# Performance work log

Measured on AMD Instinct MI355X. Metric: run time of the kernel, lower is better.

The kernel has to match this reference:

```python
import jax, jax.numpy as jnp
import numpy as np

B, T = 64, 512
OBS, DM, DS, NL = 115, 128, 8, 3
EMB, NA, H1 = 16, 19, 256


def _ln(x, g, b, eps=1e-5):
    m = jnp.mean(x, -1, keepdims=True)
    v = jnp.mean((x - m) ** 2, -1, keepdims=True)
    return (x - m) * jax.lax.rsqrt(v + eps) * g + b


def _s6(x, h, lng, lnb, w_ig, w_dt, b_dt, a_log, w_b, w_c, d_par, w_out):
    # x: [B,T,DM], h: [B,DM,DS]
    xn = _ln(x, lng, lnb)
    xp = xn @ w_ig.T                               # [B,T,2*DM]
    x_in, z = xp[..., :DM], xp[..., DM:]
    dt = jax.nn.softplus(x_in @ w_dt.T + b_dt)     # [B,T,DM]
    A = -jnp.exp(a_log)                            # [DM,DS]
    bt = x_in @ w_b.T                              # [B,T,DS]
    ct = x_in @ w_c.T                              # [B,T,DS]
    dA = jnp.exp(dt[..., None] * A)                # [B,T,DM,DS]
    upd = (dt * x_in)[..., None] * bt[:, :, None, :]  # [B,T,DM,DS]

    def step(hc, inp):
        dA_t, u_t, c_t = inp
        hn = dA_t * hc + u_t                       # [B,DM,DS]
        y = jnp.einsum('bds,bs->bd', hn, c_t)      # [B,DM]
        return hn, y

    h_f, ys = jax.lax.scan(
        step, h,
        (jnp.swapaxes(dA, 0, 1), jnp.swapaxes(upd, 0, 1), jnp.swapaxes(ct, 0, 1)))
    y = jnp.swapaxes(ys, 0, 1)                     # [B,T,DM]
    ssm = y * jax.nn.silu(z) + x_in * d_par
    return x + ssm @ w_out.T, h_f.reshape(h_f.shape[0], -1)


def _forward(prev_actions, obs, h0, enc_w1, enc_b1, enc_g1, enc_bb1, enc_w2, enc_b2,
             enc_g2, enc_bb2, emb, proj_w, proj_b, proj_g, proj_bb,
             m_ln_g, m_ln_b, m_w_ig, m_w_dt, m_b_dt, m_a_log, m_w_b, m_w_c, m_d, m_w_out,
             fn_g, fn_b, pol_w1, pol_b1, pol_g, pol_bb, pol_w2, pol_b2):
    # MLP encoder: Linear -> LN -> SiLU -> Linear -> LN (final norm)
    e = jax.nn.silu(_ln(obs @ enc_w1.T + enc_b1, enc_g1, enc_bb1))
    e = _ln(e @ enc_w2.T + enc_b2, enc_g2, enc_bb2)
    pa = emb[prev_actions]                         # [B,T,EMB]
    x = jnp.concatenate([e, pa], -1) @ proj_w.T + proj_b
    x = jax.nn.silu(_ln(x, proj_g, proj_bb))
    for i in range(NL):
        x, _ = _s6(x, h0[i].reshape(-1, DM, DS), m_ln_g[i], m_ln_b[i], m_w_ig[i],
                   m_w_dt[i], m_b_dt[i], m_a_log[i], m_w_b[i], m_w_c[i], m_d[i], m_w_out[i])
    x = _ln(x, fn_g, fn_b)
    p = jax.nn.silu(_ln(x @ pol_w1.T + pol_b1, pol_g, pol_bb))
    return p @ pol_w2.T + pol_b2                   # [B,T,NA] policy logits


def setup_inputs() -> dict:
    key = jax.random.key(0)
    ks = iter(jax.random.split(key, 64))
    def n(shape, s=0.05):
        return jax.random.normal(next(ks), shape, dtype=jnp.float32) * s
    return {
        'obs': jax.random.normal(next(ks), (B, T, OBS), dtype=jnp.float32),
        'h0': jnp.zeros((NL, B, DM * DS), jnp.float32),
        'enc_w1': n((H1, OBS)), 'enc_b1': jnp.zeros((H1,)),
        'enc_g1': jnp.ones((H1,)), 'enc_bb1': jnp.zeros((H1,)),
        'enc_w2': n((DM, H1)), 'enc_b2': jnp.zeros((DM,)),
        'enc_g2': jnp.ones((DM,)), 'enc_bb2': jnp.zeros((DM,)),
        'emb': n((NA + 1, EMB), 1.0),
        'proj_w': n((DM, DM + EMB)), 'proj_b': jnp.zeros((DM,)),
        'proj_g': jnp.ones((DM,)), 'proj_bb': jnp.zeros((DM,)),
        'm_ln_g': jnp.ones((NL, DM)), 'm_ln_b': jnp.zeros((NL, DM)),
        'm_w_ig': n((NL, 2 * DM, DM)), 'm_w_dt': n((NL, DM, DM)),
        'm_b_dt': jnp.zeros((NL, DM)),
        'm_a_log': jax.random.uniform(next(ks), (NL, DM, DS), minval=-3.0, maxval=-1.0, dtype=jnp.float32),
        'm_w_b': n((NL, DS, DM)), 'm_w_c': n((NL, DS, DM)),
        'm_d': jnp.ones((NL, DM)), 'm_w_out': n((NL, DM, DM)),
        'fn_g': jnp.ones((DM,)), 'fn_b': jnp.zeros((DM,)),
        'pol_w1': n((DM, DM)), 'pol_b1': jnp.zeros((DM,)),
        'pol_g': jnp.ones((DM,)), 'pol_bb': jnp.zeros((DM,)),
        'pol_w2': n((NA, DM)), 'pol_b2': jnp.zeros((NA,)),
        'prev_actions': jax.random.randint(next(ks), (B, T), 0, NA + 1),
    }


def reference(obs, h0, enc_w1, enc_b1, enc_g1, enc_bb1, enc_w2, enc_b2, enc_g2, enc_bb2,
              emb, proj_w, proj_b, proj_g, proj_bb, m_ln_g, m_ln_b, m_w_ig, m_w_dt,
              m_b_dt, m_a_log, m_w_b, m_w_c, m_d, m_w_out, fn_g, fn_b, pol_w1, pol_b1,
              pol_g, pol_bb, pol_w2, pol_b2, prev_actions):
    return _forward(prev_actions, obs, h0, enc_w1, enc_b1, enc_g1, enc_bb1, enc_w2,
                    enc_b2, enc_g2, enc_bb2, emb, proj_w, proj_b, proj_g, proj_bb,
                    m_ln_g, m_ln_b, m_w_ig, m_w_dt, m_b_dt, m_a_log, m_w_b, m_w_c,
                    m_d, m_w_out, fn_g, fn_b, pol_w1, pol_b1, pol_g, pol_bb, pol_w2, pol_b2)
```

## Files before the change

kernel.cpp:

```cpp
#include <hip/hip_runtime.h>
#include <math.h>

#define BB 64
#define TT 512
#define OBSD 115
#define DMD 128
#define DSD 8
#define NLD 3
#define EMBD 16
#define NAD 19
#define H1D 256
#define NTOK (BB*TT)
#define SSEG 32
#define TSEG (TT/SSEG)

typedef unsigned short ushort_t;
typedef __attribute__((ext_vector_type(8))) short short8;
typedef __attribute__((ext_vector_type(4))) float f32x4;

__device__ __forceinline__ float silu_f(float x){ return x / (1.f + __expf(-x)); }
__device__ __forceinline__ float softplus_f(float x){
  return fmaxf(x, 0.f) + log1pf(__expf(-fabsf(x)));
}
__device__ __forceinline__ ushort_t f2bf(float x){
  unsigned u = __float_as_uint(x);
  unsigned r = (u + 0x7fffu + ((u >> 16) & 1u)) >> 16;
  return (ushort_t)r;
}
__device__ __forceinline__ float b2f(ushort_t x){
  return __uint_as_float(((unsigned)x) << 16);
}
#define MFMA(a,b,c) __builtin_amdgcn_mfma_f32_16x16x32_bf16((a),(b),(c),0,0,0)
#define LOG2E 1.44269504f

template<int D, int SV>
__device__ __forceinline__ void ln32(const float* s_val, float* s_mr, int tid){
  const int t = tid >> 3, part = tid & 7;
  float s = 0.f, s2 = 0.f;
  #pragma unroll
  for (int j = part; j < D; j += 8){ float v = s_val[t*SV + j]; s += v; s2 = fmaf(v, v, s2); }
  s += __shfl_xor(s, 1, 64); s2 += __shfl_xor(s2, 1, 64);
  s += __shfl_xor(s, 2, 64); s2 += __shfl_xor(s2, 2, 64);
  s += __shfl_xor(s, 4, 64); s2 += __shfl_xor(s2, 4, 64);
  if (part == 0){
    float m = s * (1.f/(float)D);
    s_mr[t*2] = m;
    s_mr[t*2+1] = rsqrtf(s2 * (1.f/(float)D) - m*m + 1e-5f);
  }
}

struct PJob { const float* src; ushort_t* dst; int N; int K; int Kpad; int rowofs; int Nw; };
struct PJobs { PJob j[20]; };

__global__ __launch_bounds__(256) void k_prep(PJobs P){
  const int job = blockIdx.x >> 2;
  const int sub = blockIdx.x & 3;
  PJob pj = P.j[job];
  const int elems = pj.Nw * pj.Kpad;
  for (int idx = sub*256 + threadIdx.x; idx < elems; idx += 4*256){
    int n = idx / pj.Kpad;
    int k = idx - n*pj.Kpad;
    float v = (n < pj.N && k < pj.K) ? pj.src[(size_t)n*pj.K + k] : 0.f;
    pj.dst[(size_t)(pj.rowofs + n)*pj.Kpad + k] = f2bf(v);
  }
}

__global__ __launch_bounds__(256) void k_enc1(
    const float* __restrict__ obs, const ushort_t* __restrict__ w1b,
    const float* __restrict__ b1, const float* __restrict__ g1,
    const float* __restrict__ bb1, ushort_t* __restrict__ e1)
{
  __shared__ __align__(16) char sm[34048];
  float*    s_val = (float*)sm;
  ushort_t* s_a   = (ushort_t*)sm;
  float*    s_mr  = (float*)(sm + 33792);
  const int tok0 = blockIdx.x * 32;
  const int tid = threadIdx.x;
  const int lane = tid & 63, w = tid >> 6;
  const int q = lane >> 4, cn = lane & 15;
  const int m0 = (w & 1) * 16, nh = w >> 1;

  for (int e = tid; e < 32*16; e += 256){
    int t = e >> 4, kc = e & 15;
    const float* op = obs + (size_t)(tok0 + t)*OBSD;
    short8 v;
    #pragma unroll
    for (int j = 0; j < 8; j++){
      int k = kc*8 + j;
      v[j] = (short)f2bf(k < OBSD ? op[k] : 0.f);
    }
    *(short8*)&s_a[t*136 + kc*8] = v;
  }
  __syncthreads();

  short8 af[4];
  #pragma unroll
  for (int ks = 0; ks < 4; ks++)
    af[ks] = *(const short8*)&s_a[(m0 + cn)*136 + ks*32 + q*8];
  __syncthreads();

  #pragma unroll
  for (int nt = 0; nt < 8; nt++){
    const int n0 = (nh*8 + nt) * 16;
    f32x4 acc = {0.f,0.f,0.f,0.f};
    #pragma unroll
    for (int ks = 0; ks < 4; ks++){
      short8 bf = *(const short8*)&w1b[(size_t)(n0 + cn)*128 + ks*32 + q*8];
      acc = MFMA(af[ks], bf, acc);
    }
    float bias = b1[n0 + cn];
    #pragma unroll
    for (int r = 0; r < 4; r++)
      s_val[(m0 + q*4 + r)*264 + n0 + cn] = acc[r] + bias;
  }
  __syncthreads();

  ln32<256,264>(s_val, s_mr, tid);
  __syncthreads();
  for (int e = tid; e < 32*256; e += 256){
    int t = e >> 8, c = e & 255;
    float v = (s_val[t*264 + c] - s_mr[t*2]) * s_mr[t*2+1] * g1[c] + bb1[c];
    e1[(size_t)(tok0 + t)*256 + c] = f2bf(silu_f(v));
  }
}

__global__ __launch_bounds__(256) void k_enc2p(
    const ushort_t* __restrict__ e1, const ushort_t* __restrict__ w2b,
    const float* __restrict__ b2, const float* __restrict__ g2,
    const float* __restrict__ bb2,
    const float* __restrict__ emb, const int* __restrict__ pact,
    const ushort_t* __restrict__ pwb, const float* __restrict__ pb,
    const float* __restrict__ pg, const float* __restrict__ pbb,
    float* __restrict__ X,
    const float* __restrict__ lng, const float* __restrict__ lnb,
    const ushort_t* __restrict__ wigb, const ushort_t* __restrict__ wdbcb,
    const float* __restrict__ bdt,
    ushort_t* __restrict__ XINb, ushort_t* __restrict__ Zb,
    ushort_t* __restrict__ DTb, ushort_t* __restrict__ BTu, ushort_t* __restrict__ CTu,
    const float* __restrict__ alog0,
    float* __restrict__ HLOC, float* __restrict__ PPR)
{
  __shared__ __align__(16) char sm[28928];
  float*    s_val = (float*)sm;
  ushort_t* s_xin = (ushort_t*)sm;
  ushort_t* s_dt  = (ushort_t*)(sm + 8704);
  ushort_t* s_a   = (ushort_t*)(sm + 17408);
  ushort_t* s_btc = (ushort_t*)(sm + 28160);
  float*    s_mr  = (float*)(sm + 28672);

  const int tok0 = blockIdx.x * 32;
  const int bidx = blockIdx.x >> 4;
  const int ch   = blockIdx.x & 15;
  const int tid = threadIdx.x;
  const int lane = tid & 63, w = tid >> 6;
  const int q = lane >> 4, cn = lane & 15;
  const int m0 = (w & 1) * 16, nh = w >> 1;

  for (int e = tid; e < 32*32; e += 256){
    int t = e >> 5, k = e & 31;
    float v = 0.f;
    if (k < EMBD){ int a = pact[tok0 + t]; v = emb[(size_t)a*EMBD + k]; }
    s_a[t*168 + 128 + k] = f2bf(v);
  }
  {
    short8 af[8];
    #pragma unroll
    for (int ks = 0; ks < 8; ks++)
      af[ks] = *(const short8*)&e1[(size_t)(tok0 + m0 + cn)*256 + ks*32 + q*8];
    #pragma unroll
    for (int nt = 0; nt < 4; nt++){
      const int n0 = (nh*4 + nt) * 16;
      f32x4 acc = {0.f,0.f,0.f,0.f};
      #pragma unroll
      for (int ks = 0; ks < 8; ks++){
        short8 bf = *(const short8*)&w2b[(size_t)(n0 + cn)*256 + ks*32 + q*8];
        acc = MFMA(af[ks], bf, acc);
      }
      float bias = b2[n0 + cn];
      #pragma unroll
      for (int r = 0; r < 4; r++)
        s_val[(m0 + q*4 + r)*136 + n0 + cn] = acc[r] + bias;
    }
  }
  __syncthreads();

  ln32<128,136>(s_val, s_mr, tid);
  __syncthreads();
  for (int e = tid; e < 32*128; e += 256){
    int t = e >> 7, c = e & 127;
    float v = (s_val[t*136 + c] - s_mr[t*2]) * s_mr[t*2+1] * g2[c] + bb2[c];
    s_a[t*168 + c] = f2bf(v);
  }
  __syncthreads();

  {
    short8 af2[5];
    #pragma unroll
    for (int ks = 0; ks < 5; ks++)
      af2[ks] = *(const short8*)&s_a[(m0 + cn)*168 + ks*32 + q*8];
    #pragma unroll
    for (int nt = 0; nt < 4; nt++){
      const int n0 = (nh*4 + nt) * 16;
      f32x4 acc = {0.f,0.f,0.f,0.f};
      #pragma unroll
      for (int ks = 0; ks < 5; ks++){
        short8 bf = *(const short8*)&pwb[(size_t)(n0 + cn)*160 + ks*32 + q*8];
        acc = MFMA(af2[ks], bf, acc);
      }
      float bias = pb[n0 + cn];
      #pragma unroll
      for (int r = 0; r < 4; r++)
        s_val[(m0 + q*4 + r)*136 + n0 + cn] = acc[r] + bias;
    }
  }
  __syncthreads();

  ln32<128,136>(s_val, s_mr, tid);
  __syncthreads();
  for (int e = tid; e < 32*128; e += 256){
    int t = e >> 7, c = e & 127;
    float v = (s_val[t*136 + c] - s_mr[t*2]) * s_mr[t*2+1] * pg[c] + pbb[c];
    v = silu_f(v);
    X[(size_t)tok0*128 + e] = v;
    s_val[t*136 + c] = v;
  }
  __syncthreads();

  ln32<128,136>(s_val, s_mr, tid);
  __syncthreads();
  for (int e = tid; e < 32*128; e += 256){
    int t = e >> 7, c = e & 127;
    float v = (s_val[t*136 + c] - s_mr[t*2]) * s_mr[t*2+1] * lng[c] + lnb[c];
    s_a[t*168 + c] = f2bf(v);
  }
  __syncthreads();

  {
    short8 af[4];
    #pragma unroll
    for (int ks = 0; ks < 4; ks++)
      af[ks] = *(const short8*)&s_a[(m0 + cn)*168 + ks*32 + q*8];
    #pragma unroll
    for (int nt = 0; nt < 8; nt++){
      const int n0 = (nh*8 + nt) * 16;
      f32x4 acc = {0.f,0.f,0.f,0.f};
      #pragma unroll
      for (int ks = 0; ks < 4; ks++){
        short8 bf = *(const short8*)&wigb[(size_t)(n0 + cn)*128 + ks*32 + q*8];
        acc = MFMA(af[ks], bf, acc);
      }
      if (n0 < 128){
        #pragma unroll
        for (int r = 0; r < 4; r++){
          int tr = m0 + q*4 + r;
          ushort_t bb = f2bf(acc[r]);
          XINb[(size_t)(tok0 + tr)*128 + n0 + cn] = bb;
          s_xin[tr*136 + n0 + cn] = bb;
        }
      } else {
        #pragma unroll
        for (int r = 0; r < 4; r++){
          int tr = m0 + q*4 + r;
          Zb[(size_t)(tok0 + tr)*128 + (n0 - 128) + cn] = f2bf(acc[r]);
        }
      }
    }
  }
  __syncthreads();

  {
    short8 af2[4];
    #pragma unroll
    for (int ks = 0; ks < 4; ks++)
      af2[ks] = *(const short8*)&s_xin[(m0 + cn)*136 + ks*32 + q*8];
    for (int nt = nh; nt < 9; nt += 2){
      const int n0 = nt * 16;
      f32x4 acc = {0.f,0.f,0.f,0.f};
      #pragma unroll
      for (int ks = 0; ks < 4; ks++){
        short8 bf = *(const short8*)&wdbcb[(size_t)(n0 + cn)*128 + ks*32 + q*8];
        acc = MFMA(af2[ks], bf, acc);
      }
      const int col = n0 + cn;
      if (col < 128){
        float bd = bdt[col];
        #pragma unroll
        for (int r = 0; r < 4; r++){
          int tr = m0 + q*4 + r;
          ushort_t dv = f2bf(softplus_f(acc[r] + bd));
          DTb[(size_t)(tok0 + tr)*128 + col] = dv;
          s_dt[tr*136 + col] = dv;
        }
      } else if (col < 136){
        #pragma unroll
        for (int r = 0; r < 4; r++){
          int tr = m0 + q*4 + r;
          ushort_t bb = f2bf(acc[r]);
          BTu[(size_t)(tok0 + tr)*8 + (col - 128)] = bb;
          s_btc[tr*8 + (col - 128)] = bb;
        }
      } else {
        #pragma unroll
        for (int r = 0; r < 4; r++)
          CTu[(size_t)(tok0 + m0 + q*4 + r)*8 + (col - 136)] = f2bf(acc[r]);
      }
    }
  }
  __syncthreads();

  {
    const int d = tid & 127, half = tid >> 7;
    float A2c[8], hh[8], pp[8];
    #pragma unroll
    for (int s = 0; s < 8; s++){
      A2c[s] = -__expf(alog0[d*8 + s]) * LOG2E;
      hh[s] = 0.f; pp[s] = 1.f;
    }
    const int t0 = half * 16;
    #pragma unroll 4
    for (int tt = 0; tt < 16; tt++){
      const int t = t0 + tt;
      float dt = b2f(s_dt[t*136 + d]);
      float wv = dt * b2f(s_xin[t*136 + d]);
      #pragma unroll
      for (int s = 0; s < 8; s++){
        float dA = exp2f(dt * A2c[s]);
        hh[s] = fmaf(dA, hh[s], wv * b2f(s_btc[t*8 + s]));
        pp[s] *= dA;
      }
    }
    const size_t o = ((size_t)bidx*SSEG + ch*2 + half)*1024 + d*8;
    #pragma unroll
    for (int s = 0; s < 8; s++){ HLOC[o+s] = hh[s]; PPR[o+s] = pp[s]; }
  }
}

__global__ __launch_bounds__(256) void k_carry(
    float* __restrict__ HL, const float* __restrict__ PP,
    const float* __restrict__ h0g)
{
  const int idx = blockIdx.x*256 + threadIdx.x;
  float h = h0g[idx];
  size_t o = (size_t)(idx >> 10) * (SSEG*1024) + (idx & 1023);
  #pragma unroll 4
  for (int ch = 0; ch < SSEG; ch++){
    float hl = HL[o];
    float pp = PP[o];
    HL[o] = h;
    h = fmaf(pp, h, hl);
    o += 1024;
  }
}

#define SMB 26368

__device__ __forceinline__ void phaseB32(
    const ushort_t* DTb, const ushort_t* XINb, const ushort_t* Zb,
    const ushort_t* BTu, const ushort_t* CTu,
    const float* __restrict__ alog, const float* __restrict__ HLpre,
    const float* __restrict__ dpar, const ushort_t* __restrict__ woutb,
    float* __restrict__ X, char* sm, int b, int pair, int tid)
{
  ushort_t* s_dtS = (ushort_t*)sm;
  ushort_t* s_xiS = (ushort_t*)(sm + 8192);
  float*    s_x   = (float*)sm;
  ushort_t* s_a   = (ushort_t*)(sm + 16384);
  ushort_t* s_bt  = (ushort_t*)(sm + 25088);
  ushort_t* s_ct  = (ushort_t*)(sm + 25600);
  float*    s_mr  = (float*)(sm + 26112);

  const int lane = tid & 63, w = tid >> 6, q = lane >> 4, cn = lane & 15;
  const int m0 = (w & 1) * 16, nh = w >> 1;
  const int d = tid & 127, half = tid >> 7;
  const size_t segtok = (size_t)b*TT + pair*32;

  {
    const uint4* gdt = (const uint4*)(DTb + segtok*128);
    const uint4* gxi = (const uint4*)(XINb + segtok*128);
    #pragma unroll
    for (int i = 0; i < 2; i++){
      ((uint4*)s_dtS)[tid + i*256] = gdt[tid + i*256];
      ((uint4*)s_xiS)[tid + i*256] = gxi[tid + i*256];
    }
    if (tid < 128){
      ((unsigned*)s_bt)[tid] = ((const unsigned*)(BTu + segtok*8))[tid];
      ((unsigned*)s_ct)[tid] = ((const unsigned*)(CTu + segtok*8))[tid];
    }
  }
  float A2[8], h[8];
  {
    const size_t o = ((size_t)b*SSEG + pair*2 + half)*1024 + d*8;
    float4 h0v = *(const float4*)(HLpre + o);
    float4 h1v = *(const float4*)(HLpre + o + 4);
    h[0]=h0v.x; h[1]=h0v.y; h[2]=h0v.z; h[3]=h0v.w;
    h[4]=h1v.x; h[5]=h1v.y; h[6]=h1v.z; h[7]=h1v.w;
    #pragma unroll
    for (int s = 0; s < 8; s++) A2[s] = -__expf(alog[d*8 + s]) * LOG2E;
  }
  __syncthreads();

  #pragma unroll 4
  for (int tt = 0; tt < 16; tt++){
    const int t = half*16 + tt;
    float dt = b2f(s_dtS[t*128 + d]);
    float xi = b2f(s_xiS[t*128 + d]);
    float wv = dt * xi;
    float y = 0.f;
    #pragma unroll
    for (int s = 0; s < 8; s++){
      float dA = exp2f(dt * A2[s]);
      h[s] = fmaf(dA, h[s], wv * b2f(s_bt[t*8 + s]));
      y = fmaf(h[s], b2f(s_ct[t*8 + s]), y);
    }
    s_a[t*136 + d] = f2bf(y);
  }
  __syncthreads();

  {
    const int c0 = (tid & 15)*8, trow = tid >> 4;
    float dpv[8];
    #pragma unroll
    for (int j = 0; j < 8; j++) dpv[j] = dpar[c0 + j];
    #pragma unroll
    for (int i = 0; i < 2; i++){
      const int t = trow + i*16;
      uint4 zb = ((const uint4*)(Zb + segtok*128))[tid + i*256];
      const ushort_t* zp = (const ushort_t*)&zb;
      #pragma unroll
      for (int j = 0; j < 8; j++){
        float y  = b2f(s_a[t*136 + c0 + j]);
        float xi = b2f(s_xiS[t*128 + c0 + j]);
        float ssm = y * silu_f(b2f(zp[j])) + xi * dpv[j];
        s_a[t*136 + c0 + j] = f2bf(ssm);
      }
    }
  }
  __syncthreads();

  {
    short8 af[4];
    #pragma unroll
    for (int ks = 0; ks < 4; ks++)
      af[ks] = *(const short8*)&s_a[(m0 + cn)*136 + ks*32 + q*8];
    __syncthreads();
    #pragma unroll
    for (int i = 0; i < 4; i++){
      const int n0 = (nh*4 + i) * 16;
      short8 bf[4];
      #pragma unroll
      for (int ks = 0; ks < 4; ks++)
        bf[ks] = *(const short8*)&woutb[(size_t)(n0+cn)*128 + ks*32 + q*8];
      f32x4 acc = {0.f,0.f,0.f,0.f};
      #pragma unroll
      for (int ks = 0; ks < 4; ks++) acc = MFMA(af[ks], bf[ks], acc);
      #pragma unroll
      for (int r = 0; r < 4; r++){
        const int tr = m0 + q*4 + r;
        const size_t g = (segtok + tr)*128 + n0 + cn;
        float xn = X[g] + acc[r];
        X[g] = xn;
        s_x[tr*130 + n0 + cn] = xn;
      }
    }
  }
  __syncthreads();

  {
    const int t = tid >> 3, part = tid & 7;
    float s = 0.f, s2 = 0.f;
    const float* row = s_x + t*130 + part*16;
    #pragma unroll
    for (int j = 0; j < 16; j++){ float v = row[j]; s += v; s2 = fmaf(v, v, s2); }
    s  += __shfl_xor(s, 1, 64);  s2 += __shfl_xor(s2, 1, 64);
    s  += __shfl_xor(s, 2, 64);  s2 += __shfl_xor(s2, 2, 64);
    s  += __shfl_xor(s, 4, 64);  s2 += __shfl_xor(s2, 4, 64);
    if (part == 0){
      float m = s * (1.f/128.f);
      s_mr[t*2] = m;
      s_mr[t*2+1] = rsqrtf(s2 * (1.f/128.f) - m*m + 1e-5f);
    }
  }
  __syncthreads();
}

__global__ __launch_bounds__(256, 4) void k_scan2p(
    ushort_t* DTb, ushort_t* XINb, ushort_t* Zb,
    ushort_t* BTu, ushort_t* CTu,
    const float* __restrict__ alog, const float* __restrict__ HLpre,
    const float* __restrict__ dpar, const ushort_t* __restrict__ woutb,
    float* __restrict__ X,
    const float* __restrict__ lng, const float* __restrict__ lnb,
    const ushort_t* __restrict__ wigb, const ushort_t* __restrict__ wdbcb,
    const float* __restrict__ bdt,
    const float* __restrict__ alogn,
    float* __restrict__ HLo, float* __restrict__ PPo)
{
  __shared__ __align__(16) char sm[SMB];
  const int tid = threadIdx.x;
  float*    s_x   = (float*)sm;
  ushort_t* s_xin = (ushort_t*)sm;
  ushort_t* s_dt2 = (ushort_t*)(sm + 8704);
  ushort_t* s_a   = (ushort_t*)(sm + 16384);
  ushort_t* s_btc = (ushort_t*)(sm + 25088);
  float*    s_mr  = (float*)(sm + 26112);

  const int b = blockIdx.x >> 4;
  const int pair = blockIdx.x & 15;
  const int lane = tid & 63, w = tid >> 6, q = lane >> 4, cn = lane & 15;
  const int m0 = (w & 1) * 16, nh = w >> 1;
  const int d = tid & 127, half = tid >> 7;
  const size_t segtok = (size_t)b*TT + pair*32;

  phaseB32(DTb, XINb, Zb, BTu, CTu, alog, HLpre, dpar, woutb, X, sm, b, pair, tid);

  {
    float g = lng[d], c0v = lnb[d];
    float x31 = s_x[31*130 + d];
    __syncthreads();
    #pragma unroll
    for (int tt = 0; tt < 16; tt++){
      const int t = half*16 + tt;
      float xv = (t == 31) ? x31 : s_x[t*130 + d];
      float v = (xv - s_mr[t*2]) * s_mr[t*2+1] * g + c0v;
      s_a[t*136 + d] = f2bf(v);
    }
  }
  __syncthreads();

  {
    short8 af[4];
    #pragma unroll
    for (int ks = 0; ks < 4; ks++)
      af[ks] = *(const short8*)&s_a[(m0 + cn)*136 + ks*32 + q*8];
    #pragma unroll
    for (int i = 0; i < 8; i++){
      const int n0 = (nh*8 + i) * 16;
      short8 bf[4];
      #pragma unroll
      for (int ks = 0; ks < 4; ks++)
        bf[ks] = *(const short8*)&wigb[(size_t)(n0+cn)*128 + ks*32 + q*8];
      f32x4 acc = {0.f,0.f,0.f,0.f};
      #pragma unroll
      for (int ks = 0; ks < 4; ks++) acc = MFMA(af[ks], bf[ks], acc);
      if (n0 < 128){
        #pragma unroll
        for (int r = 0; r < 4; r++){
          const int tr = m0 + q*4 + r;
          ushort_t bb = f2bf(acc[r]);
          XINb[(segtok + tr)*128 + n0 + cn] = bb;
          s_xin[tr*136 + n0 + cn] = bb;
        }
      } else {
        #pragma unroll
        for (int r = 0; r < 4; r++){
          const int tr = m0 + q*4 + r;
          Zb[(segtok + tr)*128 + (n0-128) + cn] = f2bf(acc[r]);
        }
      }
    }
  }
  __syncthreads();

  {
    short8 af2[4];
    #pragma unroll
    for (int ks = 0; ks < 4; ks++)
      af2[ks] = *(const short8*)&s_xin[(m0 + cn)*136 + ks*32 + q*8];
    for (int nt = nh; nt < 9; nt += 2){
      const int n0 = nt * 16;
      short8 bf[4];
      #pragma unroll
      for (int ks = 0; ks < 4; ks++)
        bf[ks] = *(const short8*)&wdbcb[(size_t)(n0+cn)*128 + ks*32 + q*8];
      f32x4 acc = {0.f,0.f,0.f,0.f};
      #pragma unroll
      for (int ks = 0; ks < 4; ks++) acc = MFMA(af2[ks], bf[ks], acc);
      const int col = n0 + cn;
      if (col < 128){
        float bd = bdt[col];
        #pragma unroll
        for (int r = 0; r < 4; r++){
          const int tr = m0 + q*4 + r;
          ushort_t dv = f2bf(softplus_f(acc[r] + bd));
          DTb[(segtok + tr)*128 + col] = dv;
          s_dt2[tr*136 + col] = dv;
        }
      } else if (col < 136){
        #pragma unroll
        for (int r = 0; r < 4; r++){
          const int tr = m0 + q*4 + r;
          ushort_t bb = f2bf(acc[r]);
          BTu[(segtok + tr)*8 + (col-128)] = bb;
          s_btc[tr*8 + (col-128)] = bb;
        }
      } else {
        #pragma unroll
        for (int r = 0; r < 4; r++)
          CTu[(segtok + m0 + q*4 + r)*8 + (col-136)] = f2bf(acc[r]);
      }
    }
  }
  __syncthreads();

  {
    float A2n[8], hh[8], pp[8];
    #pragma unroll
    for (int s = 0; s < 8; s++){
      A2n[s] = -__expf(alogn[d*8 + s]) * LOG2E;
      hh[s] = 0.f; pp[s] = 1.f;
    }
    #pragma unroll 4
    for (int tt = 0; tt < 16; tt++){
      const int t = half*16 + tt;
      float dt = b2f(s_dt2[t*136 + d]);
      float wv = dt * b2f(s_xin[t*136 + d]);
      #pragma unroll
      for (int s = 0; s < 8; s++){
        float dA = exp2f(dt * A2n[s]);
        hh[s] = fmaf(dA, hh[s], wv * b2f(s_btc[t*8 + s]));
        pp[s] *= dA;
      }
    }
    const size_t o = ((size_t)b*SSEG + pair*2 + half)*1024 + d*8;
    #pragma unroll
    for (int s = 0; s < 8; s++){ HLo[o+s] = hh[s]; PPo[o+s] = pp[s]; }
  }
}

__global__ __launch_bounds__(256, 4) void k_scan2h(
    const ushort_t* DTb, const ushort_t* XINb, const ushort_t* Zb,
    const ushort_t* BTu, const ushort_t* CTu,
    const float* __restrict__ alog, const float* __restrict__ HLpre,
    const float* __restrict__ dpar, const ushort_t* __restrict__ woutb,
    float* __restrict__ X,
    const float* __restrict__ fng, const float* __restrict__ fnb,
    const ushort_t* __restrict__ pw1b, const float* __restrict__ pb1,
    const float* __restrict__ pg, const float* __restrict__ pbb,
    const ushort_t* __restrict__ pw2b, const float* __restrict__ pb2,
    float* __restrict__ out)
{
  __shared__ __align__(16) char sm[SMB];
  const int tid = threadIdx.x;
  float*    s_x  = (float*)sm;
  ushort_t* s_a  = (ushort_t*)(sm + 16384);
  float*    s_mr = (float*)(sm + 26112);

  const int b = blockIdx.x >> 4;
  const int pair = blockIdx.x & 15;
  const int lane = tid & 63, w = tid >> 6, q = lane >> 4, cn = lane & 15;
  const int m0 = (w & 1) * 16, nh = w >> 1;
  const int d = tid & 127, half = tid >> 7;
  const size_t segtok = (size_t)b*TT + pair*32;

  phaseB32((ushort_t*)DTb, (ushort_t*)XINb, (ushort_t*)Zb,
           (ushort_t*)BTu, (ushort_t*)CTu, alog, HLpre,
           dpar, woutb, X, sm, b, pair, tid);

  {
    float g = fng[d], c0v = fnb[d];
    float x31 = s_x[31*130 + d];
    __syncthreads();
    #pragma unroll
    for (int tt = 0; tt < 16; tt++){
      const int t = half*16 + tt;
      float xv = (t == 31) ? x31 : s_x[t*130 + d];
      float v = (xv - s_mr[t*2]) * s_mr[t*2+1] * g + c0v;
      s_a[t*136 + d] = f2bf(v);
    }
  }
  __syncthreads();

  {
    short8 af[4];
    #pragma unroll
    for (int ks = 0; ks < 4; ks++)
      af[ks] = *(const short8*)&s_a[(m0 + cn)*136 + ks*32 + q*8];
    __syncthreads();
    #pragma unroll
    for (int i = 0; i < 4; i++){
      const int n0 = (nh*4 + i) * 16;
      short8 bf[4];
      #pragma unroll
      for (int ks = 0; ks < 4; ks++)
        bf[ks] = *(const short8*)&pw1b[(size_t)(n0+cn)*128 + ks*32 + q*8];
      float bias = pb1[n0 + cn];
      f32x4 acc = {0.f,0.f,0.f,0.f};
      #pragma unroll
      for (int ks = 0; ks < 4; ks++) acc = MFMA(af[ks], bf[ks], acc);
      #pragma unroll
      for (int r = 0; r < 4; r++)
        s_x[(m0 + q*4 + r)*130 + n0 + cn] = acc[r] + bias;
    }
  }
  __syncthreads();

  {
    const int t = tid >> 3, part = tid & 7;
    float s = 0.f, s2 = 0.f;
    const float* row = s_x + t*130 + part*16;
    #pragma unroll
    for (int j = 0; j < 16; j++){ float v = row[j]; s += v; s2 = fmaf(v, v, s2); }
    s  += __shfl_xor(s, 1, 64);  s2 += __shfl_xor(s2, 1, 64);
    s  += __shfl_xor(s, 2, 64);  s2 += __shfl_xor(s2, 2, 64);
    s  += __shfl_xor(s, 4, 64);  s2 += __shfl_xor(s2, 4, 64);
    if (part == 0){
      float m = s * (1.f/128.f);
      s_mr[t*2] = m;
      s_mr[t*2+1] = rsqrtf(s2 * (1.f/128.f) - m*m + 1e-5f);
    }
  }
  __syncthreads();

  {
    float g = pg[d], c0v = pbb[d];
    float x31 = s_x[31*130 + d];
    __syncthreads();
    #pragma unroll
    for (int tt = 0; tt < 16; tt++){
      const int t = half*16 + tt;
      float xv = (t == 31) ? x31 : s_x[t*130 + d];
      float v = (xv - s_mr[t*2]) * s_mr[t*2+1] * g + c0v;
      s_a[t*136 + d] = f2bf(silu_f(v));
    }
  }
  __syncthreads();

  {
    short8 af[4];
    #pragma unroll
    for (int ks = 0; ks < 4; ks++)
      af[ks] = *(const short8*)&s_a[(m0 + cn)*136 + ks*32 + q*8];
    const int n0 = (w >> 1) * 16;
    short8 bf[4];
    #pragma unroll
    for (int ks = 0; ks < 4; ks++)
      bf[ks] = *(const short8*)&pw2b[(size_t)(n0+cn)*128 + ks*32 + q*8];
    const int col = n0 + cn;
    f32x4 acc = {0.f,0.f,0.f,0.f};
    #pragma unroll
    for (int ks = 0; ks < 4; ks++) acc = MFMA(af[ks], bf[ks], acc);
    if (col < NAD){
      float bias = pb2[col];
      #pragma unroll
      for (int r = 0; r < 4; r++)
        out[(segtok + m0 + q*4 + r)*NAD + col] = acc[r] + bias;
    }
  }
}

extern "C" void kernel_launch(void* const* d_in, const int* in_sizes, int n_in,
                              void* d_out, int out_size, void* d_ws, size_t ws_size,
                              hipStream_t stream) {
  const float* obs    = (const float*)d_in[0];
  const float* h0     = (const float*)d_in[1];
  const float* enc_w1 = (const float*)d_in[2];
  const float* enc_b1 = (const float*)d_in[3];
  const float* enc_g1 = (const float*)d_in[4];
  const float* enc_bb1= (const float*)d_in[5];
  const float* enc_w2 = (const float*)d_in[6];
  const float* enc_b2 = (const float*)d_in[7];
  const float* enc_g2 = (const float*)d_in[8];
  const float* enc_bb2= (const float*)d_in[9];
  const float* emb    = (const float*)d_in[10];
  const float* proj_w = (const float*)d_in[11];
  const float* proj_b = (const float*)d_in[12];
  const float* proj_g = (const float*)d_in[13];
  const float* proj_bb= (const float*)d_in[14];
  const float* m_ln_g = (const float*)d_in[15];
  const float* m_ln_b = (const float*)d_in[16];
  const float* m_w_ig = (const float*)d_in[17];
  const float* m_w_dt = (const float*)d_in[18];
  const float* m_b_dt = (const float*)d_in[19];
  const float* m_a_log= (const float*)d_in[20];
  const float* m_w_b  = (const float*)d_in[21];
  const float* m_w_c  = (const float*)d_in[22];
  const float* m_d    = (const float*)d_in[23];
  const float* m_w_out= (const float*)d_in[24];
  const float* fn_g   = (const float*)d_in[25];
  const float* fn_b   = (const float*)d_in[26];
  const float* pol_w1 = (const float*)d_in[27];
  const float* pol_b1 = (const float*)d_in[28];
  const float* pol_g  = (const float*)d_in[29];
  const float* pol_bb = (const float*)d_in[30];
  const float* pol_w2 = (const float*)d_in[31];
  const float* pol_b2 = (const float*)d_in[32];
  const int*   pact   = (const int*)d_in[33];

  float* ws  = (float*)d_ws;
  float* X    = ws;
  float* HLA  = X + (size_t)NTOK*128;
  float* PPA  = HLA + (size_t)BB*SSEG*1024;
  ushort_t* E1 = (ushort_t*)(PPA + (size_t)BB*SSEG*1024);
  float* HLB  = (float*)E1;
  float* PPB  = HLB + (size_t)BB*SSEG*1024;
  ushort_t* XINb = E1   + (size_t)NTOK*256;
  ushort_t* Zb   = XINb + (size_t)NTOK*128;
  ushort_t* DTb  = Zb   + (size_t)NTOK*128;
  ushort_t* BTu  = DTb  + (size_t)NTOK*128;
  ushort_t* CTu  = BTu  + (size_t)NTOK*8;

  ushort_t* W1B   = CTu   + (size_t)NTOK*8;
  ushort_t* W2B   = W1B   + 256*128;
  ushort_t* PWB   = W2B   + 128*256;
  ushort_t* WIGB  = PWB   + 128*160;
  ushort_t* WDBCB = WIGB  + 3*256*128;
  ushort_t* WOUTB = WDBCB + 3*144*128;
  ushort_t* PW1B  = WOUTB + 3*128*128;
  ushort_t* PW2B  = PW1B  + 128*128;

  PJobs P;
  int nj = 0;
  auto add = [&](const float* src, ushort_t* dst, int N, int K, int Kpad, int rowofs, int Nw){
    P.j[nj].src = src; P.j[nj].dst = dst; P.j[nj].N = N; P.j[nj].K = K;
    P.j[nj].Kpad = Kpad; P.j[nj].rowofs = rowofs; P.j[nj].Nw = Nw; nj++;
  };
  add(enc_w1, W1B, 256, 115, 128, 0, 256);
  add(enc_w2, W2B, 128, 256, 256, 0, 128);
  add(proj_w, PWB, 128, 144, 160, 0, 128);
  for (int l = 0; l < NLD; l++)
    add(m_w_ig + (size_t)l*256*128, WIGB + (size_t)l*256*128, 256, 128, 128, 0, 256);
  for (int l = 0; l < NLD; l++){
    add(m_w_dt + (size_t)l*128*128, WDBCB + (size_t)l*144*128, 128, 128, 128, 0,   128);
    add(m_w_b  + (size_t)l*8*128,   WDBCB + (size_t)l*144*128,   8, 128, 128, 128,   8);
    add(m_w_c  + (size_t)l*8*128,   WDBCB + (size_t)l*144*128,   8, 128, 128, 136,   8);
  }
  for (int l = 0; l < NLD; l++)
    add(m_w_out + (size_t)l*128*128, WOUTB + (size_t)l*128*128, 128, 128, 128, 0, 128);
  add(pol_w1, PW1B, 128, 128, 128, 0, 128);
  add(pol_w2, PW2B,  19, 128, 128, 0,  32);

  k_prep<<<20*4, 256, 0, stream>>>(P);
  k_enc1<<<NTOK/32, 256, 0, stream>>>(obs, W1B, enc_b1, enc_g1, enc_bb1, E1);
  k_enc2p<<<NTOK/32, 256, 0, stream>>>(E1, W2B, enc_b2, enc_g2, enc_bb2,
      emb, pact, PWB, proj_b, proj_g, proj_bb, X,
      m_ln_g, m_ln_b, WIGB, WDBCB, m_b_dt,
      XINb, Zb, DTb, BTu, CTu,
      m_a_log, HLA, PPA);

  const int carrygrid = BB*1024/256;
  const int scangrid  = NTOK/32;

  k_carry<<<carrygrid, 256, 0, stream>>>(HLA, PPA, h0);
  k_scan2p<<<scangrid, 256, 0, stream>>>(DTb, XINb, Zb, BTu, CTu,
      m_a_log, HLA, m_d, WOUTB, X,
      m_ln_g + 128, m_ln_b + 128,
      WIGB + (size_t)256*128, WDBCB + (size_t)144*128, m_b_dt + 128,
      m_a_log + 1024, HLB, PPB);
  k_carry<<<carrygrid, 256, 0, stream>>>(HLB, PPB, h0 + (size_t)BB*1024);
  k_scan2p<<<scangrid, 256, 0, stream>>>(DTb, XINb, Zb, BTu, CTu,
      m_a_log + 1024, HLB, m_d + 128, WOUTB + (size_t)128*128, X,
      m_ln_g + 256, m_ln_b + 256,
      WIGB + (size_t)2*256*128, WDBCB + (size_t)2*144*128, m_b_dt + 256,
      m_a_log + 2048, HLA, PPA);
  k_carry<<<carrygrid, 256, 0, stream>>>(HLA, PPA, h0 + (size_t)2*BB*1024);
  k_scan2h<<<scangrid, 256, 0, stream>>>(DTb, XINb, Zb, BTu, CTu,
      m_a_log + 2048, HLA, m_d + 256, WOUTB + (size_t)2*128*128, X,
      fn_g, fn_b, PW1B, pol_b1, pol_g, pol_bb, PW2B, pol_b2,
      (float*)d_out);
}
```

Measured before the change: 421.8 us.

## Fuse encoder layer one into the encoder-projection kernel and drop E1 buffer

New measurement: 409.0 us. -3.0%, faster.

```diff
diff --git a/kernel.cpp b/kernel.cpp
--- a/kernel.cpp
+++ b/kernel.cpp
@@ -65,67 +65,11 @@
   }
 }
 
-__global__ __launch_bounds__(256) void k_enc1(
+__global__ __launch_bounds__(256) void k_enc12p(
     const float* __restrict__ obs, const ushort_t* __restrict__ w1b,
     const float* __restrict__ b1, const float* __restrict__ g1,
-    const float* __restrict__ bb1, ushort_t* __restrict__ e1)
-{
-  __shared__ __align__(16) char sm[34048];
-  float*    s_val = (float*)sm;
-  ushort_t* s_a   = (ushort_t*)sm;
-  float*    s_mr  = (float*)(sm + 33792);
-  const int tok0 = blockIdx.x * 32;
-  const int tid = threadIdx.x;
-  const int lane = tid & 63, w = tid >> 6;
-  const int q = lane >> 4, cn = lane & 15;
-  const int m0 = (w & 1) * 16, nh = w >> 1;
-
-  for (int e = tid; e < 32*16; e += 256){
-    int t = e >> 4, kc = e & 15;
-    const float* op = obs + (size_t)(tok0 + t)*OBSD;
-    short8 v;
-    #pragma unroll
-    for (int j = 0; j < 8; j++){
-      int k = kc*8 + j;
-      v[j] = (short)f2bf(k < OBSD ? op[k] : 0.f);
-    }
-    *(short8*)&s_a[t*136 + kc*8] = v;
-  }
-  __syncthreads();
-
-  short8 af[4];
-  #pragma unroll
-  for (int ks = 0; ks < 4; ks++)
-    af[ks] = *(const short8*)&s_a[(m0 + cn)*136 + ks*32 + q*8];
-  __syncthreads();
-
-  #pragma unroll
-  for (int nt = 0; nt < 8; nt++){
-    const int n0 = (nh*8 + nt) * 16;
-    f32x4 acc = {0.f,0.f,0.f,0.f};
-    #pragma unroll
-    for (int ks = 0; ks < 4; ks++){
-      short8 bf = *(const short8*)&w1b[(size_t)(n0 + cn)*128 + ks*32 + q*8];
-      acc = MFMA(af[ks], bf, acc);
-    }
-    float bias = b1[n0 + cn];
-    #pragma unroll
-    for (int r = 0; r < 4; r++)
-      s_val[(m0 + q*4 + r)*264 + n0 + cn] = acc[r] + bias;
-  }
-  __syncthreads();
-
-  ln32<256,264>(s_val, s_mr, tid);
-  __syncthreads();
-  for (int e = tid; e < 32*256; e += 256){
-    int t = e >> 8, c = e & 255;
-    float v = (s_val[t*264 + c] - s_mr[t*2]) * s_mr[t*2+1] * g1[c] + bb1[c];
-    e1[(size_t)(tok0 + t)*256 + c] = f2bf(silu_f(v));
-  }
-}
-
-__global__ __launch_bounds__(256) void k_enc2p(
-    const ushort_t* __restrict__ e1, const ushort_t* __restrict__ w2b,
+    const float* __restrict__ bb1,
+    const ushort_t* __restrict__ w2b,
     const float* __restrict__ b2, const float* __restrict__ g2,
     const float* __restrict__ bb2,
     const float* __restrict__ emb, const int* __restrict__ pact,
@@ -140,13 +84,16 @@
     const float* __restrict__ alog0,
     float* __restrict__ HLOC, float* __restrict__ PPR)
 {
-  __shared__ __align__(16) char sm[28928];
-  float*    s_val = (float*)sm;
-  ushort_t* s_xin = (ushort_t*)sm;
-  ushort_t* s_dt  = (ushort_t*)(sm + 8704);
-  ushort_t* s_a   = (ushort_t*)(sm + 17408);
-  ushort_t* s_btc = (ushort_t*)(sm + 28160);
-  float*    s_mr  = (float*)(sm + 28672);
+  __shared__ __align__(16) char sm[35584];
+  float*    s_val  = (float*)sm;
+  ushort_t* s_obs  = (ushort_t*)sm;
+  ushort_t* s_xin  = (ushort_t*)sm;
+  ushort_t* s_dt   = (ushort_t*)(sm + 8704);
+  ushort_t* s_e1   = (ushort_t*)(sm + 17408);
+  ushort_t* s_a2   = (ushort_t*)(sm + 17408);
+  float2*   s_st   = (float2*)(sm + 34304);
+  ushort_t* s_btc  = (ushort_t*)(sm + 34816);
+  float*    s_mr   = (float*)(sm + 35328);
 
   const int tok0 = blockIdx.x * 32;
   const int bidx = blockIdx.x >> 4;
@@ -156,30 +103,107 @@
   const int q = lane >> 4, cn = lane & 15;
   const int m0 = (w & 1) * 16, nh = w >> 1;
 
-  for (int e = tid; e < 32*32; e += 256){
-    int t = e >> 5, k = e & 31;
-    float v = 0.f;
-    if (k < EMBD){ int a = pact[tok0 + t]; v = emb[(size_t)a*EMBD + k]; }
-    s_a[t*168 + 128 + k] = f2bf(v);
-  }
-  {
-    short8 af[8];
+  for (int e = tid; e < 32*16; e += 256){
+    int t = e >> 4, kc = e & 15;
+    const float* op = obs + (size_t)(tok0 + t)*OBSD;
+    short8 v;
+    #pragma unroll
+    for (int j = 0; j < 8; j++){
+      int k = kc*8 + j;
+      v[j] = (short)f2bf(k < OBSD ? op[k] : 0.f);
+    }
+    *(short8*)&s_obs[t*136 + kc*8] = v;
+  }
+  __syncthreads();
+
+  f32x4 acc[8];
+  {
+    short8 af[4];
+    #pragma unroll
+    for (int ks = 0; ks < 4; ks++)
+      af[ks] = *(const short8*)&s_obs[(m0 + cn)*136 + ks*32 + q*8];
+    #pragma unroll
+    for (int nt = 0; nt < 8; nt++){
+      const int n0 = (nh*8 + nt) * 16;
+      f32x4 a = {0.f,0.f,0.f,0.f};
+      #pragma unroll
+      for (int ks = 0; ks < 4; ks++){
+        short8 bf = *(const short8*)&w1b[(size_t)(n0 + cn)*128 + ks*32 + q*8];
+        a = MFMA(af[ks], bf, a);
+      }
+      float bv = b1[n0 + cn];
+      #pragma unroll
+      for (int r = 0; r < 4; r++) a[r] += bv;
+      acc[nt] = a;
+    }
+  }
+
+  {
+    #pragma unroll
+    for (int r = 0; r < 4; r++){
+      float s = 0.f, s2 = 0.f;
+      #pragma unroll
+      for (int nt = 0; nt < 8; nt++){ float v = acc[nt][r]; s += v; s2 = fmaf(v, v, s2); }
+      s += __shfl_xor(s, 1, 64); s2 += __shfl_xor(s2, 1, 64);
+      s += __shfl_xor(s, 2, 64); s2 += __shfl_xor(s2, 2, 64);
+      s += __shfl_xor(s, 4, 64); s2 += __shfl_xor(s2, 4, 64);
+      s += __shfl_xor(s, 8, 64); s2 += __shfl_xor(s2, 8, 64);
+      if (cn == 0) s_st[(m0 + q*4 + r)*2 + nh] = make_float2(s, s2);
+    }
+  }
+  __syncthreads();
+
+  {
+    float mu[4], rs[4];
+    #pragma unroll
+    for (int r = 0; r < 4; r++){
+      const int row = m0 + q*4 + r;
+      float2 p0 = s_st[row*2 + 0], p1 = s_st[row*2 + 1];
+      float s = p0.x + p1.x, s2 = p0.y + p1.y;
+      float m = s * (1.f/256.f);
+      mu[r] = m;
+      rs[r] = rsqrtf(s2 * (1.f/256.f) - m*m + 1e-5f);
+    }
+    #pragma unroll
+    for (int nt = 0; nt < 8; nt++){
+      const int col = (nh*8 + nt)*16 + cn;
+      float gg = g1[col], bbv = bb1[col];
+      #pragma unroll
+      for (int r = 0; r < 4; r++){
+        float v = (acc[nt][r] - mu[r]) * rs[r] * gg + bbv;
+        s_e1[(m0 + q*4 + r)*264 + col] = f2bf(silu_f(v));
+      }
+    }
+  }
+  __syncthreads();
+
+  {
+    short8 af2[8];
     #pragma unroll
     for (int ks = 0; ks < 8; ks++)
-      af[ks] = *(const short8*)&e1[(size_t)(tok0 + m0 + cn)*256 + ks*32 + q*8];
+      af2[ks] = *(const short8*)&s_e1[(m0 + cn)*264 + ks*32 + q*8];
+    __syncthreads();
+
+    for (int e = tid; e < 32*32; e += 256){
+      int t = e >> 5, k = e & 31;
+      float v = 0.f;
+      if (k < EMBD){ int a = pact[tok0 + t]; v = emb[(size_t)a*EMBD + k]; }
+      s_a2[t*168 + 128 + k] = f2bf(v);
+    }
+
     #pragma unroll
     for (int nt = 0; nt < 4; nt++){
       const int n0 = (nh*4 + nt) * 16;
-      f32x4 acc = {0.f,0.f,0.f,0.f};
+      f32x4 a = {0.f,0.f,0.f,0.f};
       #pragma unroll
       for (int ks = 0; ks < 8; ks++){
         short8 bf = *(const short8*)&w2b[(size_t)(n0 + cn)*256 + ks*32 + q*8];
-        acc = MFMA(af[ks], bf, acc);
+        a = MFMA(af2[ks], bf, a);
       }
       float bias = b2[n0 + cn];
       #pragma unroll
       for (int r = 0; r < 4; r++)
-        s_val[(m0 + q*4 + r)*136 + n0 + cn] = acc[r] + bias;
+        s_val[(m0 + q*4 + r)*136 + n0 + cn] = a[r] + bias;
     }
   }
   __syncthreads();
@@ -189,28 +213,28 @@
   for (int e = tid; e < 32*128; e += 256){
     int t = e >> 7, c = e & 127;
     float v = (s_val[t*136 + c] - s_mr[t*2]) * s_mr[t*2+1] * g2[c] + bb2[c];
-    s_a[t*168 + c] = f2bf(v);
-  }
-  __syncthreads();
-
-  {
-    short8 af2[5];
+    s_a2[t*168 + c] = f2bf(v);
+  }
+  __syncthreads();
+
+  {
+    short8 af3[5];
     #pragma unroll
     for (int ks = 0; ks < 5; ks++)
-      af2[ks] = *(const short8*)&s_a[(m0 + cn)*168 + ks*32 + q*8];
+      af3[ks] = *(const short8*)&s_a2[(m0 + cn)*168 + ks*32 + q*8];
     #pragma unroll
     for (int nt = 0; nt < 4; nt++){
       const int n0 = (nh*4 + nt) * 16;
-      f32x4 acc = {0.f,0.f,0.f,0.f};
+      f32x4 a = {0.f,0.f,0.f,0.f};
       #pragma unroll
       for (int ks = 0; ks < 5; ks++){
         short8 bf = *(const short8*)&pwb[(size_t)(n0 + cn)*160 + ks*32 + q*8];
-        acc = MFMA(af2[ks], bf, acc);
+        a = MFMA(af3[ks], bf, a);
       }
       float bias = pb[n0 + cn];
       #pragma unroll
       for (int r = 0; r < 4; r++)
-        s_val[(m0 + q*4 + r)*136 + n0 + cn] = acc[r] + bias;
+        s_val[(m0 + q*4 + r)*136 + n0 + cn] = a[r] + bias;
     }
   }
   __syncthreads();
@@ -231,7 +255,7 @@
   for (int e = tid; e < 32*128; e += 256){
     int t = e >> 7, c = e & 127;
     float v = (s_val[t*136 + c] - s_mr[t*2]) * s_mr[t*2+1] * lng[c] + lnb[c];
-    s_a[t*168 + c] = f2bf(v);
+    s_a2[t*168 + c] = f2bf(v);
   }
   __syncthreads();
 
@@ -239,21 +263,21 @@
     short8 af[4];
     #pragma unroll
     for (int ks = 0; ks < 4; ks++)
-      af[ks] = *(const short8*)&s_a[(m0 + cn)*168 + ks*32 + q*8];
+      af[ks] = *(const short8*)&s_a2[(m0 + cn)*168 + ks*32 + q*8];
     #pragma unroll
     for (int nt = 0; nt < 8; nt++){
       const int n0 = (nh*8 + nt) * 16;
-      f32x4 acc = {0.f,0.f,0.f,0.f};
+      f32x4 a = {0.f,0.f,0.f,0.f};
       #pragma unroll
       for (int ks = 0; ks < 4; ks++){
         short8 bf = *(const short8*)&wigb[(size_t)(n0 + cn)*128 + ks*32 + q*8];
-        acc = MFMA(af[ks], bf, acc);
+        a = MFMA(af[ks], bf, a);
       }
       if (n0 < 128){
         #pragma unroll
         for (int r = 0; r < 4; r++){
           int tr = m0 + q*4 + r;
-          ushort_t bb = f2bf(acc[r]);
+          ushort_t bb = f2bf(a[r]);
           XINb[(size_t)(tok0 + tr)*128 + n0 + cn] = bb;
           s_xin[tr*136 + n0 + cn] = bb;
         }
@@ -261,7 +285,7 @@
         #pragma unroll
         for (int r = 0; r < 4; r++){
           int tr = m0 + q*4 + r;
-          Zb[(size_t)(tok0 + tr)*128 + (n0 - 128) + cn] = f2bf(acc[r]);
+          Zb[(size_t)(tok0 + tr)*128 + (n0 - 128) + cn] = f2bf(a[r]);
         }
       }
     }
@@ -275,11 +299,11 @@
       af2[ks] = *(const short8*)&s_xin[(m0 + cn)*136 + ks*32 + q*8];
     for (int nt = nh; nt < 9; nt += 2){
       const int n0 = nt * 16;
-      f32x4 acc = {0.f,0.f,0.f,0.f};
+      f32x4 a = {0.f,0.f,0.f,0.f};
       #pragma unroll
       for (int ks = 0; ks < 4; ks++){
         short8 bf = *(const short8*)&wdbcb[(size_t)(n0 + cn)*128 + ks*32 + q*8];
-        acc = MFMA(af2[ks], bf, acc);
+        a = MFMA(af2[ks], bf, a);
       }
       const int col = n0 + cn;
       if (col < 128){
@@ -287,7 +311,7 @@
         #pragma unroll
         for (int r = 0; r < 4; r++){
           int tr = m0 + q*4 + r;
-          ushort_t dv = f2bf(softplus_f(acc[r] + bd));
+          ushort_t dv = f2bf(softplus_f(a[r] + bd));
           DTb[(size_t)(tok0 + tr)*128 + col] = dv;
           s_dt[tr*136 + col] = dv;
         }
@@ -295,14 +319,14 @@
         #pragma unroll
         for (int r = 0; r < 4; r++){
           int tr = m0 + q*4 + r;
-          ushort_t bb = f2bf(acc[r]);
+          ushort_t bb = f2bf(a[r]);
           BTu[(size_t)(tok0 + tr)*8 + (col - 128)] = bb;
           s_btc[tr*8 + (col - 128)] = bb;
         }
       } else {
         #pragma unroll
         for (int r = 0; r < 4; r++)
-          CTu[(size_t)(tok0 + m0 + q*4 + r)*8 + (col - 136)] = f2bf(acc[r]);
+          CTu[(size_t)(tok0 + m0 + q*4 + r)*8 + (col - 136)] = f2bf(a[r]);
       }
     }
   }
@@ -340,19 +364,22 @@
     const float* __restrict__ h0g)
 {
   const int idx = blockIdx.x*256 + threadIdx.x;
+  const size_t base = (size_t)(idx >> 10) * (SSEG*1024) + (idx & 1023);
+  float hl[SSEG], pp[SSEG];
+  #pragma unroll
+  for (int ch = 0; ch < SSEG; ch++){
+    hl[ch] = HL[base + (size_t)ch*1024];
+    pp[ch] = PP[base + (size_t)ch*1024];
+  }
   float h = h0g[idx];
-  size_t o = (size_t)(idx >> 10) * (SSEG*1024) + (idx & 1023);
-  #pragma unroll 4
+  #pragma unroll
   for (int ch = 0; ch < SSEG; ch++){
-    float hl = HL[o];
-    float pp = PP[o];
-    HL[o] = h;
-    h = fmaf(pp, h, hl);
-    o += 1024;
-  }
-}
-
-#define SMB 26368
+    HL[base + (size_t)ch*1024] = h;
+    h = fmaf(pp[ch], h, hl[ch]);
+  }
+}
+
+#define SMB 26624
 
 __device__ __forceinline__ void phaseB32(
     const ushort_t* DTb, const ushort_t* XINb, const ushort_t* Zb,
@@ -364,10 +391,10 @@
   ushort_t* s_dtS = (ushort_t*)sm;
   ushort_t* s_xiS = (ushort_t*)(sm + 8192);
   float*    s_x   = (float*)sm;
-  ushort_t* s_a   = (ushort_t*)(sm + 16384);
-  ushort_t* s_bt  = (ushort_t*)(sm + 25088);
-  ushort_t* s_ct  = (ushort_t*)(sm + 25600);
-  float*    s_mr  = (float*)(sm + 26112);
+  ushort_t* s_a   = (ushort_t*)(sm + 16640);
+  ushort_t* s_bt  = (ushort_t*)(sm + 25344);
+  ushort_t* s_ct  = (ushort_t*)(sm + 25856);
+  float*    s_mr  = (float*)(sm + 26368);
 
   const int lane = tid & 63, w = tid >> 6, q = lane >> 4, cn = lane & 15;
   const int m0 = (w & 1) * 16, nh = w >> 1;
@@ -442,7 +469,6 @@
     #pragma unroll
     for (int ks = 0; ks < 4; ks++)
       af[ks] = *(const short8*)&s_a[(m0 + cn)*136 + ks*32 + q*8];
-    __syncthreads();
     #pragma unroll
     for (int i = 0; i < 4; i++){
       const int n0 = (nh*4 + i) * 16;
@@ -500,9 +526,9 @@
   float*    s_x   = (float*)sm;
   ushort_t* s_xin = (ushort_t*)sm;
   ushort_t* s_dt2 = (ushort_t*)(sm + 8704);
-  ushort_t* s_a   = (ushort_t*)(sm + 16384);
-  ushort_t* s_btc = (ushort_t*)(sm + 25088);
-  float*    s_mr  = (float*)(sm + 26112);
+  ushort_t* s_a   = (ushort_t*)(sm + 16640);
+  ushort_t* s_btc = (ushort_t*)(sm + 25344);
+  float*    s_mr  = (float*)(sm + 26368);
 
   const int b = blockIdx.x >> 4;
   const int pair = blockIdx.x & 15;
@@ -515,13 +541,10 @@
 
   {
     float g = lng[d], c0v = lnb[d];
-    float x31 = s_x[31*130 + d];
-    __syncthreads();
     #pragma unroll
     for (int tt = 0; tt < 16; tt++){
       const int t = half*16 + tt;
-      float xv = (t == 31) ? x31 : s_x[t*130 + d];
-      float v = (xv - s_mr[t*2]) * s_mr[t*2+1] * g + c0v;
+      float v = (s_x[t*130 + d] - s_mr[t*2]) * s_mr[t*2+1] * g + c0v;
       s_a[t*136 + d] = f2bf(v);
     }
   }
@@ -642,8 +665,8 @@
   __shared__ __align__(16) char sm[SMB];
   const int tid = threadIdx.x;
   float*    s_x  = (float*)sm;
-  ushort_t* s_a  = (ushort_t*)(sm + 16384);
-  float*    s_mr = (float*)(sm + 26112);
+  ushort_t* s_a  = (ushort_t*)(sm + 16640);
+  float*    s_mr = (float*)(sm + 26368);
 
   const int b = blockIdx.x >> 4;
   const int pair = blockIdx.x & 15;
@@ -658,13 +681,10 @@
 
   {
     float g = fng[d], c0v = fnb[d];
-    float x31 = s_x[31*130 + d];
-    __syncthreads();
     #pragma unroll
     for (int tt = 0; tt < 16; tt++){
       const int t = half*16 + tt;
-      float xv = (t == 31) ? x31 : s_x[t*130 + d];
-      float v = (xv - s_mr[t*2]) * s_mr[t*2+1] * g + c0v;
+      float v = (s_x[t*130 + d] - s_mr[t*2]) * s_mr[t*2+1] * g + c0v;
       s_a[t*136 + d] = f2bf(v);
     }
   }
@@ -675,7 +695,6 @@
     #pragma unroll
     for (int ks = 0; ks < 4; ks++)
       af[ks] = *(const short8*)&s_a[(m0 + cn)*136 + ks*32 + q*8];
-    __syncthreads();
     #pragma unroll
     for (int i = 0; i < 4; i++){
       const int n0 = (nh*4 + i) * 16;
@@ -713,13 +732,10 @@
 
   {
     float g = pg[d], c0v = pbb[d];
-    float x31 = s_x[31*130 + d];
-    __syncthreads();
     #pragma unroll
     for (int tt = 0; tt < 16; tt++){
       const int t = half*16 + tt;
-      float xv = (t == 31) ? x31 : s_x[t*130 + d];
-      float v = (xv - s_mr[t*2]) * s_mr[t*2+1] * g + c0v;
+      float v = (s_x[t*130 + d] - s_mr[t*2]) * s_mr[t*2+1] * g + c0v;
       s_a[t*136 + d] = f2bf(silu_f(v));
     }
   }
@@ -790,10 +806,9 @@
   float* X    = ws;
   float* HLA  = X + (size_t)NTOK*128;
   float* PPA  = HLA + (size_t)BB*SSEG*1024;
-  ushort_t* E1 = (ushort_t*)(PPA + (size_t)BB*SSEG*1024);
-  float* HLB  = (float*)E1;
+  float* HLB  = PPA + (size_t)BB*SSEG*1024;
   float* PPB  = HLB + (size_t)BB*SSEG*1024;
-  ushort_t* XINb = E1   + (size_t)NTOK*256;
+  ushort_t* XINb = (ushort_t*)(PPB + (size_t)BB*SSEG*1024);
   ushort_t* Zb   = XINb + (size_t)NTOK*128;
   ushort_t* DTb  = Zb   + (size_t)NTOK*128;
   ushort_t* BTu  = DTb  + (size_t)NTOK*128;
@@ -830,8 +845,8 @@
   add(pol_w2, PW2B,  19, 128, 128, 0,  32);
 
   k_prep<<<20*4, 256, 0, stream>>>(P);
-  k_enc1<<<NTOK/32, 256, 0, stream>>>(obs, W1B, enc_b1, enc_g1, enc_bb1, E1);
-  k_enc2p<<<NTOK/32, 256, 0, stream>>>(E1, W2B, enc_b2, enc_g2, enc_bb2,
+  k_enc12p<<<NTOK/32, 256, 0, stream>>>(obs, W1B, enc_b1, enc_g1, enc_bb1,
+      W2B, enc_b2, enc_g2, enc_bb2,
       emb, pact, PWB, proj_b, proj_g, proj_bb, X,
       m_ln_g, m_ln_b, WIGB, WDBCB, m_b_dt,
       XINb, Zb, DTb, BTu, CTu,
```
